# Kernel tuning notes

Hardware: AMD Instinct MI355X
Metric: run time of the kernel (lower is better)

## Reference

```python
import jax, jax.numpy as jnp
import numpy as np

N = 50000      # nodes
E = 800000     # edges (avg degree 16)
F_IN = 32
H = 64         # hidden_features
E_DIM = 16     # edge_dim
C_OUT = 40
L = 2          # num_layers
G = 64         # graphs in batch
BN_EPS = 1e-5
GEN_EPS = 1e-7  # PyG GENConv message eps


def setup_inputs() -> dict:
    key = jax.random.key(0)
    ks = jax.random.split(key, 12)
    s = 0.05
    inp = {}
    inp["x"] = jax.random.normal(ks[0], (N, F_IN), jnp.float32)
    inp["edge_index"] = jax.random.randint(ks[1], (2, E), 0, N)
    inp["edge_attr"] = jax.random.normal(ks[2], (E, E_DIM), jnp.float32)
    inp["batch"] = jnp.sort(jax.random.randint(ks[3], (N,), 0, G))
    # input linear
    inp["lin_in_w"] = jax.random.normal(ks[4], (F_IN, H), jnp.float32) * s
    inp["lin_in_b"] = jnp.zeros((H,), jnp.float32)
    # per-layer DeepGCNLayer norm (BatchNorm affine)
    inp["norm_gamma"] = jnp.ones((L, H), jnp.float32)
    inp["norm_beta"] = jnp.zeros((L, H), jnp.float32)
    # per-layer GENConv params
    inp["edge_w"] = jax.random.normal(ks[5], (L, E_DIM, H), jnp.float32) * s
    inp["edge_b"] = jnp.zeros((L, H), jnp.float32)
    inp["t"] = jnp.ones((L,), jnp.float32)  # learned softmax temperature
    inp["mlp_w1"] = jax.random.normal(ks[6], (L, H, 2 * H), jnp.float32) * s
    inp["mlp_b1"] = jnp.zeros((L, 2 * H), jnp.float32)
    inp["mlp_gamma"] = jnp.ones((L, 2 * H), jnp.float32)
    inp["mlp_beta"] = jnp.zeros((L, 2 * H), jnp.float32)
    inp["mlp_w2"] = jax.random.normal(ks[7], (L, 2 * H, H), jnp.float32) * s
    inp["mlp_b2"] = jnp.zeros((L, H), jnp.float32)
    # output linear
    inp["lin_out_w"] = jax.random.normal(ks[8], (H, C_OUT), jnp.float32) * s
    inp["lin_out_b"] = jnp.zeros((C_OUT,), jnp.float32)
    return inp


def _batch_norm(x, gamma, beta):
    mu = jnp.mean(x, axis=0)
    var = jnp.var(x, axis=0)
    return (x - mu) * jax.lax.rsqrt(var + BN_EPS) * gamma + beta


def _gen_conv(x, src, dst, e_emb, t, w1, b1, g1, be1, w2, b2):
    # message: relu(x_j + edge_emb) + eps   -> [E, H]
    m = jax.nn.relu(x[src] + e_emb) + GEN_EPS
    # softmax aggregation over destination neighborhoods with temperature t
    logits = m * t
    seg_max = jax.ops.segment_max(logits, dst, num_segments=N)      # [N, H]
    ex = jnp.exp(logits - seg_max[dst])                              # [E, H]
    denom = jax.ops.segment_sum(ex, dst, num_segments=N)            # [N, H]
    agg = jax.ops.segment_sum(ex * m, dst, num_segments=N) / (denom + 1e-16)
    # root add, then GENConv MLP: Linear(H,2H) -> BN -> ReLU -> Linear(2H,H)
    out = agg + x
    h = out @ w1 + b1
    h = jax.nn.relu(_batch_norm(h, g1, be1))
    return h @ w2 + b2


def reference(x, edge_index, edge_attr, batch, lin_in_w, lin_in_b,
              norm_gamma, norm_beta, edge_w, edge_b, t,
              mlp_w1, mlp_b1, mlp_gamma, mlp_beta, mlp_w2, mlp_b2,
              lin_out_w, lin_out_b):
    src, dst = edge_index[0], edge_index[1]
    h = x @ lin_in_w + lin_in_b                                      # [N, H]
    for l in range(L):
        # DeepGCNLayer res+ : norm -> act -> (dropout p=0) -> conv, residual add
        z = jax.nn.relu(_batch_norm(h, norm_gamma[l], norm_beta[l]))
        e_emb = edge_attr @ edge_w[l] + edge_b[l]                    # [E, H]
        c = _gen_conv(z, src, dst, e_emb, t[l], mlp_w1[l], mlp_b1[l],
                      mlp_gamma[l], mlp_beta[l], mlp_w2[l], mlp_b2[l])
        h = h + c
    # global mean pool per graph
    sums = jax.ops.segment_sum(h, batch, num_segments=G)             # [G, H]
    counts = jax.ops.segment_sum(jnp.ones((N, 1), h.dtype), batch, num_segments=G)
    pooled = sums / jnp.maximum(counts, 1.0)
    out = jax.nn.relu(pooled) @ lin_out_w + lin_out_b                # [G, C_OUT]
    return out
```

## Files before the change

kernel.cpp:

```cpp
#include <hip/hip_runtime.h>

#define N_NODES 50000
#define N_EDGES 800000
#define F_INP   32
#define HDIM    64
#define EDIM    16
#define COUT    40
#define NGRAPH  64

__global__ void hist_kernel(const int* __restrict__ dst, int* __restrict__ cnt, int E) {
    int e = blockIdx.x * 256 + threadIdx.x;
    if (e < E) atomicAdd(&cnt[dst[e]], 1);
}

__global__ void scan_part_kernel(const int* __restrict__ cnt, int* __restrict__ bsum, int n) {
    __shared__ int red[256];
    int tid = threadIdx.x;
    int idx = blockIdx.x * 256 + tid;
    red[tid] = (idx < n) ? cnt[idx] : 0;
    __syncthreads();
    for (int off = 128; off > 0; off >>= 1) {
        if (tid < off) red[tid] += red[tid + off];
        __syncthreads();
    }
    if (tid == 0) bsum[blockIdx.x] = red[0];
}

__global__ void scan_top_kernel(int* __restrict__ bsum, int nb) {
    __shared__ int tmp[256];
    int tid = threadIdx.x;
    int v = (tid < nb) ? bsum[tid] : 0;
    tmp[tid] = v;
    __syncthreads();
    for (int off = 1; off < 256; off <<= 1) {
        int x = (tid >= off) ? tmp[tid - off] : 0;
        __syncthreads();
        tmp[tid] += x;
        __syncthreads();
    }
    if (tid < nb) bsum[tid] = tmp[tid] - v;
}

__global__ void scan_apply_kernel(const int* __restrict__ cnt, const int* __restrict__ bsum,
                                  int* __restrict__ offsets, int* __restrict__ cursor, int n) {
    __shared__ int tmp[256];
    int tid = threadIdx.x;
    int idx = blockIdx.x * 256 + tid;
    int v = (idx < n) ? cnt[idx] : 0;
    tmp[tid] = v;
    __syncthreads();
    for (int off = 1; off < 256; off <<= 1) {
        int x = (tid >= off) ? tmp[tid - off] : 0;
        __syncthreads();
        tmp[tid] += x;
        __syncthreads();
    }
    int excl = tmp[tid] - v + bsum[blockIdx.x];
    if (idx < n) { offsets[idx] = excl; cursor[idx] = excl; }
    if (idx == n - 1) offsets[n] = excl + v;
}

__global__ void scatter_kernel(const int* __restrict__ dst, const int* __restrict__ src,
                               int* __restrict__ cursor, int* __restrict__ sorted,
                               int* __restrict__ dsts, int* __restrict__ srcs, int E) {
    int e = blockIdx.x * 256 + threadIdx.x;
    if (e < E) {
        int d = dst[e];
        int p = atomicAdd(&cursor[d], 1);
        sorted[p] = e;
        dsts[p]   = d;
        srcs[p]   = src[e];
    }
}

__global__ void gstart_kernel(const int* __restrict__ batch, int* __restrict__ gstart,
                              int N, int G) {
    int n = blockIdx.x * 256 + threadIdx.x;
    if (n >= N) return;
    int g  = batch[n];
    int gp = (n == 0) ? -1 : batch[n - 1];
    for (int gg = gp + 1; gg <= g; gg++) gstart[gg] = n;
    if (n == N - 1) {
        for (int gg = g + 1; gg <= G; gg++) gstart[gg] = N;
    }
}

__global__ void lin_in_kernel(const float* __restrict__ x, const float* __restrict__ W,
                              const float* __restrict__ b, float* __restrict__ h, int N) {
    int tid = threadIdx.x;
    int c = tid & 63;
    float w[F_INP];
#pragma unroll
    for (int k = 0; k < F_INP; k++) w[k] = W[k * HDIM + c];
    int node = blockIdx.x * 4 + (tid >> 6);
    if (node >= N) return;
    const float4* xr = (const float4*)(x + (size_t)node * F_INP);
    float acc = b[c];
#pragma unroll
    for (int k4 = 0; k4 < F_INP / 4; k4++) {
        float4 xv = xr[k4];
        acc += xv.x * w[k4 * 4 + 0] + xv.y * w[k4 * 4 + 1]
             + xv.z * w[k4 * 4 + 2] + xv.w * w[k4 * 4 + 3];
    }
    h[(size_t)node * HDIM + c] = acc;
}

template <int C>
__global__ void bn_stats_kernel(const float* __restrict__ x, float* __restrict__ stats, int N) {
    const int RPB = 256 / C;
    int tid = threadIdx.x;
    int c = tid % C;
    int row0 = blockIdx.x * RPB + tid / C;
    int stride = gridDim.x * RPB;
    float s = 0.f, ss = 0.f;
    for (int r = row0; r < N; r += stride) {
        float v = x[(size_t)r * C + c];
        s += v; ss += v * v;
    }
    __shared__ float ls[256], lss[256];
    ls[tid] = s; lss[tid] = ss;
    __syncthreads();
    if (tid < C) {
        for (int k = 1; k < RPB; k++) { s += ls[tid + k * C]; ss += lss[tid + k * C]; }
        atomicAdd(&stats[c], s);
        atomicAdd(&stats[C + c], ss);
    }
}

__global__ __launch_bounds__(256) void edge_agg_kernel(
        const float* __restrict__ h, const float* __restrict__ ea,
        const int* __restrict__ sorted, const int* __restrict__ dsts,
        const int* __restrict__ srcs,
        const float* __restrict__ We, const float* __restrict__ be,
        const float* __restrict__ tptr, const float* __restrict__ stats,
        const float* __restrict__ gamma, const float* __restrict__ beta,
        float* __restrict__ num, float* __restrict__ den) {
    int tid = threadIdx.x;
    int c  = tid & 63;
    int wv = tid >> 6;
    float inv = 1.0f / (float)N_NODES;
    float mu  = stats[c] * inv;
    float var = stats[HDIM + c] * inv - mu * mu;
    float sc  = rsqrtf(var + 1e-5f) * gamma[c];
    float sb  = beta[c] - mu * sc;
    float w[EDIM];
#pragma unroll
    for (int k = 0; k < EDIM; k++) w[k] = We[k * HDIM + c];
    float bc = be[c];
    float tval = *tptr;

    int p = (blockIdx.x * 4 + wv) * 64 + c;
    int d_own = dsts[p];
    int s_own = srcs[p];
    int e     = sorted[p];
    float a[EDIM];
    {
        const float4* ar = (const float4*)(ea + (size_t)e * EDIM);
        float4 a0 = ar[0], a1 = ar[1], a2 = ar[2], a3 = ar[3];
        a[0]=a0.x; a[1]=a0.y; a[2]=a0.z; a[3]=a0.w;
        a[4]=a1.x; a[5]=a1.y; a[6]=a1.z; a[7]=a1.w;
        a[8]=a2.x; a[9]=a2.y; a[10]=a2.z; a[11]=a2.w;
        a[12]=a3.x; a[13]=a3.y; a[14]=a3.z; a[15]=a3.w;
    }

    float nacc = 0.f, dacc = 0.f;
    int cur_d = __builtin_amdgcn_readlane(d_own, 0);
    for (int jj = 0; jj < 64; jj += 8) {
        float hv[8];
#pragma unroll
        for (int u = 0; u < 8; u++) {
            int su = __builtin_amdgcn_readlane(s_own, jj + u);
            hv[u] = h[(size_t)su * HDIM + c];
        }
#pragma unroll
        for (int u = 0; u < 8; u++) {
            int du = __builtin_amdgcn_readlane(d_own, jj + u);
            if (du != cur_d) {
                atomicAdd(&num[(size_t)cur_d * HDIM + c], nacc);
                atomicAdd(&den[(size_t)cur_d * HDIM + c], dacc);
                nacc = 0.f; dacc = 0.f;
                cur_d = du;
            }
            float acc = bc;
#pragma unroll
            for (int k = 0; k < EDIM; k++) {
                float ak = __uint_as_float(
                    __builtin_amdgcn_readlane(__float_as_uint(a[k]), jj + u));
                acc += ak * w[k];
            }
            float zv = fmaxf(hv[u] * sc + sb, 0.f);
            float m  = fmaxf(zv + acc, 0.f) + 1e-7f;
            float ex = __expf(m * tval);
            dacc += ex;
            nacc += ex * m;
        }
    }
    atomicAdd(&num[(size_t)cur_d * HDIM + c], nacc);
    atomicAdd(&den[(size_t)cur_d * HDIM + c], dacc);
}

__global__ __launch_bounds__(256) void mlp1_kernel(
        float* __restrict__ num, float* __restrict__ den,
        const float* __restrict__ h, const float* __restrict__ stats,
        const float* __restrict__ gamma, const float* __restrict__ beta,
        const float* __restrict__ W1, const float* __restrict__ b1,
        float* __restrict__ h1, int N) {
    __shared__ float sW[HDIM * 128];
    __shared__ float srow[32 * 65];
    int tid = threadIdx.x;
    for (int i = tid; i < HDIM * 128; i += 256) sW[i] = W1[i];
    int base = blockIdx.x * 32;
    {
        int cc = tid & 63;
        float inv = 1.0f / (float)N_NODES;
        float mu  = stats[cc] * inv;
        float var = stats[HDIM + cc] * inv - mu * mu;
        float rs  = rsqrtf(var + 1e-5f);
        float ga  = gamma[cc], bb = beta[cc];
        for (int i = tid; i < 32 * HDIM; i += 256) {
            int r = i >> 6;
            int node = base + r;
            float v = 0.f;
            if (node < N) {
                size_t idx = (size_t)node * HDIM + cc;
                float hv = h[idx];
                float z  = fmaxf((hv - mu) * rs * ga + bb, 0.f);
                float nu = num[idx], de = den[idx];
                num[idx] = 0.f; den[idx] = 0.f;
                v = nu / (de + 1e-16f) + z;
            }
            srow[r * 65 + cc] = v;
        }
    }
    __syncthreads();
    int tx = tid & 31;
    int ty = tid >> 5;
    float acc[4][4];
    float b0 = b1[4 * tx], bb1 = b1[4 * tx + 1], b2v = b1[4 * tx + 2], b3 = b1[4 * tx + 3];
#pragma unroll
    for (int j = 0; j < 4; j++) { acc[j][0] = b0; acc[j][1] = bb1; acc[j][2] = b2v; acc[j][3] = b3; }
#pragma unroll 8
    for (int k = 0; k < HDIM; k++) {
        float4 wv = *(const float4*)&sW[k * 128 + 4 * tx];
        float r0 = srow[(ty * 4 + 0) * 65 + k];
        float r1 = srow[(ty * 4 + 1) * 65 + k];
        float r2 = srow[(ty * 4 + 2) * 65 + k];
        float r3 = srow[(ty * 4 + 3) * 65 + k];
        acc[0][0] += r0 * wv.x; acc[0][1] += r0 * wv.y; acc[0][2] += r0 * wv.z; acc[0][3] += r0 * wv.w;
        acc[1][0] += r1 * wv.x; acc[1][1] += r1 * wv.y; acc[1][2] += r1 * wv.z; acc[1][3] += r1 * wv.w;
        acc[2][0] += r2 * wv.x; acc[2][1] += r2 * wv.y; acc[2][2] += r2 * wv.z; acc[2][3] += r2 * wv.w;
        acc[3][0] += r3 * wv.x; acc[3][1] += r3 * wv.y; acc[3][2] += r3 * wv.z; acc[3][3] += r3 * wv.w;
    }
#pragma unroll
    for (int j = 0; j < 4; j++) {
        int node = base + ty * 4 + j;
        if (node < N)
            *(float4*)&h1[(size_t)node * 128 + 4 * tx] =
                make_float4(acc[j][0], acc[j][1], acc[j][2], acc[j][3]);
    }
}

__global__ __launch_bounds__(256) void mlp2_kernel(
        const float* __restrict__ h1, const float* __restrict__ stats,
        const float* __restrict__ mg, const float* __restrict__ mb,
        const float* __restrict__ W2, const float* __restrict__ b2,
        float* __restrict__ h, int N) {
    __shared__ float sW[128 * HDIM];
    __shared__ float sact[32 * 129];
    __shared__ float sbn[4 * 128];
    int tid = threadIdx.x;
    for (int i = tid; i < 128 * HDIM; i += 256) sW[i] = W2[i];
    if (tid < 128) {
        float inv = 1.0f / (float)N;
        float mu  = stats[tid] * inv;
        float var = stats[128 + tid] * inv - mu * mu;
        sbn[tid]       = mu;
        sbn[128 + tid] = rsqrtf(var + 1e-5f);
        sbn[256 + tid] = mg[tid];
        sbn[384 + tid] = mb[tid];
    }
    __syncthreads();
    int base = blockIdx.x * 32;
    for (int i = tid; i < 32 * 128; i += 256) {
        int r = i >> 7, o = i & 127;
        int node = base + r;
        float v = 0.f;
        if (node < N) {
            v = h1[(size_t)node * 128 + o];
            v = fmaxf((v - sbn[o]) * sbn[128 + o] * sbn[256 + o] + sbn[384 + o], 0.f);
        }
        sact[r * 129 + o] = v;
    }
    __syncthreads();
    int tx = tid & 15;
    int ty = tid >> 4;
    float acc[2][4];
    float b0 = b2[4 * tx], bb1 = b2[4 * tx + 1], b2v = b2[4 * tx + 2], b3 = b2[4 * tx + 3];
    acc[0][0] = b0; acc[0][1] = bb1; acc[0][2] = b2v; acc[0][3] = b3;
    acc[1][0] = b0; acc[1][1] = bb1; acc[1][2] = b2v; acc[1][3] = b3;
#pragma unroll 8
    for (int k = 0; k < 128; k++) {
        float4 wv = *(const float4*)&sW[k * HDIM + 4 * tx];
        float r0 = sact[(ty * 2 + 0) * 129 + k];
        float r1 = sact[(ty * 2 + 1) * 129 + k];
        acc[0][0] += r0 * wv.x; acc[0][1] += r0 * wv.y; acc[0][2] += r0 * wv.z; acc[0][3] += r0 * wv.w;
        acc[1][0] += r1 * wv.x; acc[1][1] += r1 * wv.y; acc[1][2] += r1 * wv.z; acc[1][3] += r1 * wv.w;
    }
#pragma unroll
    for (int j = 0; j < 2; j++) {
        int node = base + ty * 2 + j;
        if (node < N) {
            float4* p = (float4*)&h[(size_t)node * HDIM + 4 * tx];
            float4 old = *p;
            *p = make_float4(old.x + acc[j][0], old.y + acc[j][1],
                             old.z + acc[j][2], old.w + acc[j][3]);
        }
    }
}

__global__ void pool_out_kernel(const float* __restrict__ h, const int* __restrict__ gstart,
                                const float* __restrict__ Wo, const float* __restrict__ bo,
                                float* __restrict__ out, int N) {
    __shared__ float sp[HDIM];
    __shared__ float red[256];
    __shared__ float sW[HDIM * COUT];
    int g = blockIdx.x;
    int tid = threadIdx.x;
    for (int i = tid; i < HDIM * COUT; i += 256) sW[i] = Wo[i];
    int beg = gstart[g], end = gstart[g + 1];
    int c = tid & 63, r0 = tid >> 6;
    float s = 0.f;
    for (int r = beg + r0; r < end; r += 4) s += h[(size_t)r * HDIM + c];
    red[tid] = s;
    __syncthreads();
    if (tid < HDIM) {
        s = red[tid] + red[tid + 64] + red[tid + 128] + red[tid + 192];
        float cnt = (float)(end - beg);
        float pooled = s / fmaxf(cnt, 1.0f);
        sp[tid] = fmaxf(pooled, 0.0f);
    }
    __syncthreads();
    if (tid < COUT) {
        float acc = bo[tid];
#pragma unroll
        for (int k = 0; k < HDIM; k++) acc += sp[k] * sW[k * COUT + tid];
        out[g * COUT + tid] = acc;
    }
}

extern "C" void kernel_launch(void* const* d_in, const int* in_sizes, int n_in,
                              void* d_out, int out_size, void* d_ws, size_t ws_size,
                              hipStream_t stream) {
    (void)in_sizes; (void)n_in; (void)out_size; (void)ws_size;
    const float* x          = (const float*)d_in[0];
    const int*   eidx       = (const int*)  d_in[1];
    const float* eattr      = (const float*)d_in[2];
    const int*   batch      = (const int*)  d_in[3];
    const float* lin_in_w   = (const float*)d_in[4];
    const float* lin_in_b   = (const float*)d_in[5];
    const float* norm_gamma = (const float*)d_in[6];
    const float* norm_beta  = (const float*)d_in[7];
    const float* edge_w     = (const float*)d_in[8];
    const float* edge_b     = (const float*)d_in[9];
    const float* tparam     = (const float*)d_in[10];
    const float* mlp_w1     = (const float*)d_in[11];
    const float* mlp_b1     = (const float*)d_in[12];
    const float* mlp_gamma  = (const float*)d_in[13];
    const float* mlp_beta   = (const float*)d_in[14];
    const float* mlp_w2     = (const float*)d_in[15];
    const float* mlp_b2     = (const float*)d_in[16];
    const float* lin_out_w  = (const float*)d_in[17];
    const float* lin_out_b  = (const float*)d_in[18];
    float* out = (float*)d_out;

    const int* src = eidx;
    const int* dst = eidx + N_EDGES;

    char* ws = (char*)d_ws;
    size_t off = 0;
    auto alloc = [&](size_t bytes) -> char* {
        char* p = ws + off;
        off = (off + bytes + 255) & ~(size_t)255;
        return p;
    };
    int*   cnt     = (int*)  alloc((size_t)N_NODES * 4);
    float* statsA0 = (float*)alloc(128 * 4);
    float* statsB0 = (float*)alloc(256 * 4);
    float* statsA1 = (float*)alloc(128 * 4);
    float* statsB1 = (float*)alloc(256 * 4);
    size_t zero_bytes = off;
    int*   bsum    = (int*)  alloc(256 * 4);
    int*   offsets = (int*)  alloc((size_t)(N_NODES + 1) * 4);
    int*   cursor  = (int*)  alloc((size_t)N_NODES * 4);
    int*   sorted  = (int*)  alloc((size_t)N_EDGES * 4);
    int*   dsts    = (int*)  alloc((size_t)N_EDGES * 4);
    int*   srcs    = (int*)  alloc((size_t)N_EDGES * 4);
    int*   gstart  = (int*)  alloc((size_t)(NGRAPH + 1) * 4);
    float* h       = (float*)alloc((size_t)N_NODES * HDIM * 4);
    float* num     = (float*)alloc((size_t)N_NODES * HDIM * 4);
    float* den     = (float*)alloc((size_t)N_NODES * HDIM * 4);
    float* h1      = (float*)alloc((size_t)N_NODES * 2 * HDIM * 4);

    hipMemsetAsync(d_ws, 0, zero_bytes, stream);
    hipMemsetAsync(num, 0, (size_t)N_NODES * HDIM * 4 * 2, stream);

    const int NB = (N_NODES + 255) / 256;
    hist_kernel      <<<(N_EDGES + 255) / 256, 256, 0, stream>>>(dst, cnt, N_EDGES);
    scan_part_kernel <<<NB, 256, 0, stream>>>(cnt, bsum, N_NODES);
    scan_top_kernel  <<<1, 256, 0, stream>>>(bsum, NB);
    scan_apply_kernel<<<NB, 256, 0, stream>>>(cnt, bsum, offsets, cursor, N_NODES);
    scatter_kernel   <<<(N_EDGES + 255) / 256, 256, 0, stream>>>(dst, src, cursor, sorted, dsts, srcs, N_EDGES);
    gstart_kernel    <<<NB, 256, 0, stream>>>(batch, gstart, N_NODES, NGRAPH);
    lin_in_kernel    <<<(N_NODES + 3) / 4, 256, 0, stream>>>(x, lin_in_w, lin_in_b, h, N_NODES);

    const int AGG_BLOCKS = N_EDGES / 256;

    float* statsA[2] = { statsA0, statsA1 };
    float* statsB[2] = { statsB0, statsB1 };
    for (int l = 0; l < 2; l++) {
        bn_stats_kernel<64><<<256, 256, 0, stream>>>(h, statsA[l], N_NODES);
        edge_agg_kernel<<<AGG_BLOCKS, 256, 0, stream>>>(
            h, eattr, sorted, dsts, srcs,
            edge_w + (size_t)l * EDIM * HDIM, edge_b + l * HDIM,
            tparam + l, statsA[l], norm_gamma + l * HDIM, norm_beta + l * HDIM,
            num, den);
        mlp1_kernel<<<(N_NODES + 31) / 32, 256, 0, stream>>>(
            num, den, h, statsA[l], norm_gamma + l * HDIM, norm_beta + l * HDIM,
            mlp_w1 + (size_t)l * HDIM * 2 * HDIM, mlp_b1 + l * 2 * HDIM, h1, N_NODES);
        bn_stats_kernel<128><<<256, 256, 0, stream>>>(h1, statsB[l], N_NODES);
        mlp2_kernel<<<(N_NODES + 31) / 32, 256, 0, stream>>>(
            h1, statsB[l], mlp_gamma + l * 2 * HDIM, mlp_beta + l * 2 * HDIM,
            mlp_w2 + (size_t)l * 2 * HDIM * HDIM, mlp_b2 + l * HDIM, h, N_NODES);
    }
    pool_out_kernel<<<NGRAPH, 256, 0, stream>>>(h, gstart, lin_out_w, lin_out_b, out, N_NODES);
}
```

Measured before the change: 706.1 us.

## Fuse BatchNorm statistics into producer kernels and drop bn_stats launches

Removes the separate bn_stats kernels and computes per-channel sum and sum-of-squares as an epilogue in the kernels that write the tensors: lin_in for layer-0 stats, mlp1 for the hidden MLP stats, and mlp2 for the next layer's input stats. This avoids re-reading the h and h1 arrays from memory and saves four kernel launches. In exchange, mlp1 and mlp2 gain extra shared-memory reductions and many more global atomics, since there are about 1563 blocks instead of 256. lin_in becomes a grid-stride kernel with 256 blocks.

```diff
diff --git a/kernel.cpp b/kernel.cpp
--- a/kernel.cpp
+++ b/kernel.cpp
@@ -85,45 +85,37 @@
     }
 }
 
-__global__ void lin_in_kernel(const float* __restrict__ x, const float* __restrict__ W,
-                              const float* __restrict__ b, float* __restrict__ h, int N) {
+__global__ __launch_bounds__(256) void lin_in_kernel(
+        const float* __restrict__ x, const float* __restrict__ W,
+        const float* __restrict__ b, float* __restrict__ h,
+        float* __restrict__ stats, int N) {
     int tid = threadIdx.x;
     int c = tid & 63;
     float w[F_INP];
 #pragma unroll
     for (int k = 0; k < F_INP; k++) w[k] = W[k * HDIM + c];
-    int node = blockIdx.x * 4 + (tid >> 6);
-    if (node >= N) return;
-    const float4* xr = (const float4*)(x + (size_t)node * F_INP);
-    float acc = b[c];
-#pragma unroll
-    for (int k4 = 0; k4 < F_INP / 4; k4++) {
-        float4 xv = xr[k4];
-        acc += xv.x * w[k4 * 4 + 0] + xv.y * w[k4 * 4 + 1]
-             + xv.z * w[k4 * 4 + 2] + xv.w * w[k4 * 4 + 3];
-    }
-    h[(size_t)node * HDIM + c] = acc;
-}
-
-template <int C>
-__global__ void bn_stats_kernel(const float* __restrict__ x, float* __restrict__ stats, int N) {
-    const int RPB = 256 / C;
-    int tid = threadIdx.x;
-    int c = tid % C;
-    int row0 = blockIdx.x * RPB + tid / C;
-    int stride = gridDim.x * RPB;
+    float bcv = b[c];
     float s = 0.f, ss = 0.f;
-    for (int r = row0; r < N; r += stride) {
-        float v = x[(size_t)r * C + c];
-        s += v; ss += v * v;
+    for (int node = blockIdx.x * 4 + (tid >> 6); node < N; node += 1024) {
+        const float4* xr = (const float4*)(x + (size_t)node * F_INP);
+        float acc = bcv;
+#pragma unroll
+        for (int k4 = 0; k4 < F_INP / 4; k4++) {
+            float4 xv = xr[k4];
+            acc += xv.x * w[k4 * 4 + 0] + xv.y * w[k4 * 4 + 1]
+                 + xv.z * w[k4 * 4 + 2] + xv.w * w[k4 * 4 + 3];
+        }
+        h[(size_t)node * HDIM + c] = acc;
+        s += acc; ss += acc * acc;
     }
     __shared__ float ls[256], lss[256];
     ls[tid] = s; lss[tid] = ss;
     __syncthreads();
-    if (tid < C) {
-        for (int k = 1; k < RPB; k++) { s += ls[tid + k * C]; ss += lss[tid + k * C]; }
-        atomicAdd(&stats[c], s);
-        atomicAdd(&stats[C + c], ss);
+    if (tid < 64) {
+        float ts  = ls[tid] + ls[tid + 64] + ls[tid + 128] + ls[tid + 192];
+        float tss = lss[tid] + lss[tid + 64] + lss[tid + 128] + lss[tid + 192];
+        atomicAdd(&stats[c], ts);
+        atomicAdd(&stats[HDIM + c], tss);
     }
 }
 
@@ -204,7 +196,7 @@
         const float* __restrict__ h, const float* __restrict__ stats,
         const float* __restrict__ gamma, const float* __restrict__ beta,
         const float* __restrict__ W1, const float* __restrict__ b1,
-        float* __restrict__ h1, int N) {
+        float* __restrict__ h1, float* __restrict__ statsB, int N) {
     __shared__ float sW[HDIM * 128];
     __shared__ float srow[32 * 65];
     int tid = threadIdx.x;
@@ -251,12 +243,34 @@
         acc[2][0] += r2 * wv.x; acc[2][1] += r2 * wv.y; acc[2][2] += r2 * wv.z; acc[2][3] += r2 * wv.w;
         acc[3][0] += r3 * wv.x; acc[3][1] += r3 * wv.y; acc[3][2] += r3 * wv.z; acc[3][3] += r3 * wv.w;
     }
+    float ps[4] = {0.f,0.f,0.f,0.f}, pq[4] = {0.f,0.f,0.f,0.f};
 #pragma unroll
     for (int j = 0; j < 4; j++) {
         int node = base + ty * 4 + j;
-        if (node < N)
+        if (node < N) {
             *(float4*)&h1[(size_t)node * 128 + 4 * tx] =
                 make_float4(acc[j][0], acc[j][1], acc[j][2], acc[j][3]);
+#pragma unroll
+            for (int q = 0; q < 4; q++) { ps[q] += acc[j][q]; pq[q] += acc[j][q] * acc[j][q]; }
+        }
+    }
+    __syncthreads();
+    float* sredS = &srow[0];
+    float* sredQ = &srow[1024];
+    int sl = (tx * 8 + ty) * 4;
+#pragma unroll
+    for (int q = 0; q < 4; q++) { sredS[sl + q] = ps[q]; sredQ[sl + q] = pq[q]; }
+    __syncthreads();
+    if (tid < 128) {
+        int txx = tid >> 2, q = tid & 3;
+        float s2 = 0.f, q2 = 0.f;
+#pragma unroll
+        for (int t2 = 0; t2 < 8; t2++) {
+            s2 += sredS[(txx * 8 + t2) * 4 + q];
+            q2 += sredQ[(txx * 8 + t2) * 4 + q];
+        }
+        atomicAdd(&statsB[tid], s2);
+        atomicAdd(&statsB[128 + tid], q2);
     }
 }
 
@@ -264,7 +278,7 @@
         const float* __restrict__ h1, const float* __restrict__ stats,
         const float* __restrict__ mg, const float* __restrict__ mb,
         const float* __restrict__ W2, const float* __restrict__ b2,
-        float* __restrict__ h, int N) {
+        float* __restrict__ h, float* __restrict__ statsNext, int N) {
     __shared__ float sW[128 * HDIM];
     __shared__ float sact[32 * 129];
     __shared__ float sbn[4 * 128];
@@ -306,14 +320,40 @@
         acc[0][0] += r0 * wv.x; acc[0][1] += r0 * wv.y; acc[0][2] += r0 * wv.z; acc[0][3] += r0 * wv.w;
         acc[1][0] += r1 * wv.x; acc[1][1] += r1 * wv.y; acc[1][2] += r1 * wv.z; acc[1][3] += r1 * wv.w;
     }
+    float ps[4] = {0.f,0.f,0.f,0.f}, pq[4] = {0.f,0.f,0.f,0.f};
 #pragma unroll
     for (int j = 0; j < 2; j++) {
         int node = base + ty * 2 + j;
         if (node < N) {
             float4* p = (float4*)&h[(size_t)node * HDIM + 4 * tx];
             float4 old = *p;
-            *p = make_float4(old.x + acc[j][0], old.y + acc[j][1],
-                             old.z + acc[j][2], old.w + acc[j][3]);
+            float n0 = old.x + acc[j][0], n1 = old.y + acc[j][1];
+            float n2 = old.z + acc[j][2], n3 = old.w + acc[j][3];
+            *p = make_float4(n0, n1, n2, n3);
+            ps[0] += n0; pq[0] += n0 * n0;
+            ps[1] += n1; pq[1] += n1 * n1;
+            ps[2] += n2; pq[2] += n2 * n2;
+            ps[3] += n3; pq[3] += n3 * n3;
+        }
+    }
+    if (statsNext) {
+        __syncthreads();
+        float* sredS = &sact[0];
+        float* sredQ = &sact[1024];
+        int sl = (tx * 16 + ty) * 4;
+#pragma unroll
+        for (int q = 0; q < 4; q++) { sredS[sl + q] = ps[q]; sredQ[sl + q] = pq[q]; }
+        __syncthreads();
+        if (tid < 64) {
+            int txx = tid >> 2, q = tid & 3;
+            float s2 = 0.f, q2 = 0.f;
+#pragma unroll
+            for (int t2 = 0; t2 < 16; t2++) {
+                s2 += sredS[(txx * 16 + t2) * 4 + q];
+                q2 += sredQ[(txx * 16 + t2) * 4 + q];
+            }
+            atomicAdd(&statsNext[tid], s2);
+            atomicAdd(&statsNext[HDIM + tid], q2);
         }
     }
 }
@@ -411,14 +451,13 @@
     scan_apply_kernel<<<NB, 256, 0, stream>>>(cnt, bsum, offsets, cursor, N_NODES);
     scatter_kernel   <<<(N_EDGES + 255) / 256, 256, 0, stream>>>(dst, src, cursor, sorted, dsts, srcs, N_EDGES);
     gstart_kernel    <<<NB, 256, 0, stream>>>(batch, gstart, N_NODES, NGRAPH);
-    lin_in_kernel    <<<(N_NODES + 3) / 4, 256, 0, stream>>>(x, lin_in_w, lin_in_b, h, N_NODES);
+    lin_in_kernel    <<<256, 256, 0, stream>>>(x, lin_in_w, lin_in_b, h, statsA0, N_NODES);
 
     const int AGG_BLOCKS = N_EDGES / 256;
 
     float* statsA[2] = { statsA0, statsA1 };
     float* statsB[2] = { statsB0, statsB1 };
     for (int l = 0; l < 2; l++) {
-        bn_stats_kernel<64><<<256, 256, 0, stream>>>(h, statsA[l], N_NODES);
         edge_agg_kernel<<<AGG_BLOCKS, 256, 0, stream>>>(
             h, eattr, sorted, dsts, srcs,
             edge_w + (size_t)l * EDIM * HDIM, edge_b + l * HDIM,
@@ -426,11 +465,12 @@
             num, den);
         mlp1_kernel<<<(N_NODES + 31) / 32, 256, 0, stream>>>(
             num, den, h, statsA[l], norm_gamma + l * HDIM, norm_beta + l * HDIM,
-            mlp_w1 + (size_t)l * HDIM * 2 * HDIM, mlp_b1 + l * 2 * HDIM, h1, N_NODES);
-        bn_stats_kernel<128><<<256, 256, 0, stream>>>(h1, statsB[l], N_NODES);
+            mlp_w1 + (size_t)l * HDIM * 2 * HDIM, mlp_b1 + l * 2 * HDIM, h1,
+            statsB[l], N_NODES);
         mlp2_kernel<<<(N_NODES + 31) / 32, 256, 0, stream>>>(
             h1, statsB[l], mlp_gamma + l * 2 * HDIM, mlp_beta + l * 2 * HDIM,
-            mlp_w2 + (size_t)l * 2 * HDIM * HDIM, mlp_b2 + l * HDIM, h, N_NODES);
+            mlp_w2 + (size_t)l * 2 * HDIM * HDIM, mlp_b2 + l * HDIM, h,
+            (l == 0) ? statsA1 : (float*)nullptr, N_NODES);
     }
     pool_out_kernel<<<NGRAPH, 256, 0, stream>>>(h, gstart, lin_out_w, lin_out_b, out, N_NODES);
 }
```

Result: no change. 715.1 us (+1.3%).
